# Kernel tuning notes

Measured on AMD Instinct MI355X. Metric: run time of the kernel, lower is better.

## Reference

```python
import jax, jax.numpy as jnp
import numpy as np

NUM_HEADS = 16

def setup_inputs() -> dict:
    key = jax.random.key(0)
    ks = jax.random.split(key, 5)
    b, n, d = 2, 2048, 1024
    s = 0.02
    return {
        "x": jax.random.normal(ks[0], (b, n, d), jnp.float32),
        "wq": jax.random.normal(ks[1], (d, d), jnp.float32) * s,
        "wk": jax.random.normal(ks[2], (d, d), jnp.float32) * s,
        "wv": jax.random.normal(ks[3], (d, d), jnp.float32) * s,
        "wo": jax.random.normal(ks[4], (d, d), jnp.float32) * s,
        "bo": jnp.zeros((d,), jnp.float32),
    }

def reference(x, wq, wk, wv, wo, bo):
    b, n, c = x.shape
    h = NUM_HEADS
    hd = c // h
    scale = hd ** -0.5
    # qkv projections (qkv_bias=False); torch Linear computes x @ W.T
    def split_heads(t):
        return t.reshape(b, n, h, hd).transpose(0, 2, 1, 3)  # b h n d
    q = split_heads(x @ wq.T)
    k = split_heads(x @ wk.T)
    v = split_heads(x @ wv.T)
    dots = jnp.einsum('bhid,bhjd->bhij', q, k) * scale
    attn = jax.nn.softmax(dots, axis=-1)  # attn_drop=0 -> identity
    out = jnp.einsum('bhij,bhjd->bhid', attn, v)
    out = out.transpose(0, 2, 1, 3).reshape(b, n, c)
    out = out @ wo.T + bo  # proj_drop=0 -> identity
    return out
```

## Files before the change

kernel.cpp:

```cpp
#include <hip/hip_runtime.h>
#include <hip/hip_bf16.h>

typedef float f32x4 __attribute__((ext_vector_type(4)));
typedef short short8 __attribute__((ext_vector_type(8)));
typedef short short4v __attribute__((ext_vector_type(4)));

#define MFMA(a, b, c) __builtin_amdgcn_mfma_f32_16x16x32_bf16((a), (b), (c), 0, 0, 0)

#if __has_builtin(__builtin_amdgcn_mfma_f32_16x16x16_bf16)
#define MFMA16(a, b, c) __builtin_amdgcn_mfma_f32_16x16x16_bf16((a), (b), (c), 0, 0, 0)
#elif __has_builtin(__builtin_amdgcn_mfma_f32_16x16x16bf16_1k)
#define MFMA16(a, b, c) __builtin_amdgcn_mfma_f32_16x16x16bf16_1k((a), (b), (c), 0, 0, 0)
#else
static __device__ __forceinline__ f32x4 mfma16_asm(short4v a, short4v b, f32x4 c) {
    asm volatile("v_mfma_f32_16x16x16_bf16 %0, %1, %2, %0" : "+v"(c) : "v"(a), "v"(b));
    return c;
}
#define MFMA16(a, b, c) mfma16_asm((a), (b), (c))
#endif

#if __has_builtin(__builtin_amdgcn_exp2f)
#define EXP2(x) __builtin_amdgcn_exp2f(x)
#else
#define EXP2(x) exp2f(x)
#endif

#define B_  2
#define N_  2048
#define C_  1024
#define H_  16
#define HD_ 64
#define M_  (B_ * N_)

#define QSCALE 0.18033688011112042f

typedef const __attribute__((address_space(1))) void* gp_t;
typedef __attribute__((address_space(3))) void* sp_t;
#define GLL16(g, s) __builtin_amdgcn_global_load_lds((gp_t)(const void*)(g), (sp_t)(void*)(s), 16, 0, 0)

__device__ __forceinline__ short f2bf(float f) {
    union { float fv; unsigned u; } v; v.fv = f;
    unsigned r = v.u + 0x7fffu + ((v.u >> 16) & 1u);
    return (short)(r >> 16);
}
__device__ __forceinline__ unsigned pack_rne(float a, float b) {
    return (unsigned)(unsigned short)f2bf(a) | ((unsigned)(unsigned short)f2bf(b) << 16);
}

__global__ __launch_bounds__(256) void convert_kernel(
    const float* __restrict__ x,  const float* __restrict__ wq,
    const float* __restrict__ wk, const float* __restrict__ wv,
    const float* __restrict__ wo, short* __restrict__ dst)
{
    size_t e = ((size_t)blockIdx.x * 256 + threadIdx.x) * 8;
    const float* src; size_t off;
    if (e < 4194304)      { src = x;  off = e; }
    else if (e < 5242880) { src = wq; off = e - 4194304; }
    else if (e < 6291456) { src = wk; off = e - 5242880; }
    else if (e < 7340032) { src = wv; off = e - 6291456; }
    else                  { src = wo; off = e - 7340032; }
    float4 a = *(const float4*)(src + off);
    float4 b = *(const float4*)(src + off + 4);
    short8 s;
    s[0] = f2bf(a.x); s[1] = f2bf(a.y); s[2] = f2bf(a.z); s[3] = f2bf(a.w);
    s[4] = f2bf(b.x); s[5] = f2bf(b.y); s[6] = f2bf(b.z); s[7] = f2bf(b.w);
    *(short8*)(dst + e) = s;
}

__global__ __launch_bounds__(256) void qkv_gemm(
    const short* __restrict__ xb, const short* __restrict__ Wb,
    short* __restrict__ Qb, short* __restrict__ Kb, short* __restrict__ Vt)
{
    const int m0 = blockIdx.x * 128;
    const int n0 = blockIdx.y * 128;
    __shared__ short As[128 * 32];
    __shared__ short Bs[128 * 32];
    const int tid  = threadIdx.x;
    const int wave = tid >> 6, lane = tid & 63;
    const int quad = lane >> 4, l16 = lane & 15;
    const int wr = (wave >> 1) * 64, wc = (wave & 1) * 64;

    f32x4 acc[4][4] = {};

    for (int kk = 0; kk < C_; kk += 32) {
        __syncthreads();
        #pragma unroll
        for (int it = 0; it < 2; ++it) {
            int f = (it * 256 + tid) * 8;
            int row = f >> 5, col = f & 31;
            GLL16(xb + (size_t)(m0 + row) * C_ + kk + col, &As[f]);
            GLL16(Wb + (size_t)(n0 + row) * C_ + kk + col, &Bs[f]);
        }
        __syncthreads();
        short8 af[4], bf[4];
        #pragma unroll
        for (int mi = 0; mi < 4; ++mi) af[mi] = *(const short8*)&As[(wr + mi * 16 + l16) * 32 + quad * 8];
        #pragma unroll
        for (int ni = 0; ni < 4; ++ni) bf[ni] = *(const short8*)&Bs[(wc + ni * 16 + l16) * 32 + quad * 8];
        #pragma unroll
        for (int mi = 0; mi < 4; ++mi)
        #pragma unroll
        for (int ni = 0; ni < 4; ++ni)
            acc[mi][ni] = MFMA(af[mi], bf[ni], acc[mi][ni]);
    }

    const int which = n0 >> 10;
    const int nb = n0 & 1023;
    #pragma unroll
    for (int mi = 0; mi < 4; ++mi)
    #pragma unroll
    for (int ni = 0; ni < 4; ++ni)
    #pragma unroll
    for (int r = 0; r < 4; ++r) {
        int m  = m0 + wr + mi * 16 + quad * 4 + r;
        int cc = nb + wc + ni * 16 + l16;
        float av = acc[mi][ni][r];
        if (which == 0) av *= QSCALE;
        short bv = f2bf(av);
        int b = m >> 11, ns = m & (N_ - 1);
        int h = cc >> 6, d = cc & 63;
        size_t bh = (size_t)(b * H_ + h);
        if (which == 0)      Qb[(bh * N_ + ns) * HD_ + d] = bv;
        else if (which == 1) Kb[(bh * N_ + ns) * HD_ + d] = bv;
        else                 Vt[(bh * HD_ + d) * N_ + ns] = bv;
    }
}

__global__ __launch_bounds__(256, 2) void attn_kernel(
    const short* __restrict__ Qb, const short* __restrict__ Kb,
    const short* __restrict__ Vt, short* __restrict__ Ob)
{
    const int bh = blockIdx.y;
    const int b = bh >> 4, h = bh & (H_ - 1);
    const int i0 = blockIdx.x * 128;
    __shared__ short Qs[128 * 72];
    __shared__ short Ks[64 * 72];
    __shared__ short Vs[64 * 72];
    const int tid  = threadIdx.x;
    const int wave = tid >> 6, lane = tid & 63;
    const int quad = lane >> 4, l16 = lane & 15;

    const short* Qg = Qb + ((size_t)bh * N_ + i0) * HD_;
    const short* Kg = Kb + (size_t)bh * N_ * HD_;
    const short* Vg = Vt + (size_t)bh * HD_ * N_;

    #pragma unroll
    for (int it = 0; it < 4; ++it) {
        int e = tid + it * 256;
        int row = e >> 3, c8 = e & 7;
        *(uint4*)&Qs[row * 72 + c8 * 8] = *(const uint4*)(Qg + row * HD_ + c8 * 8);
    }
    __syncthreads();
    short8 qf[2][2];
    #pragma unroll
    for (int s = 0; s < 2; ++s) {
        qf[s][0] = *(const short8*)&Qs[(wave * 32 + s * 16 + l16) * 72 +      quad * 8];
        qf[s][1] = *(const short8*)&Qs[(wave * 32 + s * 16 + l16) * 72 + 32 + quad * 8];
    }

    f32x4 o[2][4] = {};
    float lrow[2] = {0.f, 0.f};

    for (int j0 = 0; j0 < N_; j0 += 64) {
        __syncthreads();
        #pragma unroll
        for (int it = 0; it < 2; ++it) {
            int e = tid + it * 256;
            int row = e >> 3, c8 = e & 7;
            *(uint4*)&Ks[row * 72 + c8 * 8] = *(const uint4*)(Kg + (size_t)(j0 + row) * HD_ + c8 * 8);
            *(uint4*)&Vs[row * 72 + c8 * 8] = *(const uint4*)(Vg + (size_t)row * N_ + j0 + c8 * 8);
        }
        __syncthreads();

        #pragma unroll
        for (int ni = 0; ni < 4; ++ni) {
            short8 kf0 = *(const short8*)&Ks[(ni * 16 + l16) * 72 +      quad * 8];
            short8 kf1 = *(const short8*)&Ks[(ni * 16 + l16) * 72 + 32 + quad * 8];
            short4v pp[2];
            #pragma unroll
            for (int s = 0; s < 2; ++s) {
                f32x4 st = {0.f, 0.f, 0.f, 0.f};
                st = MFMA(kf0, qf[s][0], st);
                st = MFMA(kf1, qf[s][1], st);
                union { float f; unsigned u; } c0, c1, c2, c3;
                c0.f = EXP2(st[0]); c1.f = EXP2(st[1]);
                c2.f = EXP2(st[2]); c3.f = EXP2(st[3]);
                lrow[s] += (c0.f + c1.f) + (c2.f + c3.f);
                unsigned w0 = (c0.u >> 16) | (c1.u & 0xffff0000u);
                unsigned w1 = (c2.u >> 16) | (c3.u & 0xffff0000u);
                union { unsigned u[2]; short4v s4; } pk;
                pk.u[0] = w0; pk.u[1] = w1;
                pp[s] = pk.s4;
            }
            #pragma unroll
            for (int di = 0; di < 4; ++di) {
                short4v vf = *(const short4v*)&Vs[(di * 16 + l16) * 72 + ni * 16 + quad * 4];
                o[0][di] = MFMA16(vf, pp[0], o[0][di]);
                o[1][di] = MFMA16(vf, pp[1], o[1][di]);
            }
        }
    }

    #pragma unroll
    for (int s = 0; s < 2; ++s) {
        float l = lrow[s];
        l += __shfl_xor(l, 16, 64);
        l += __shfl_xor(l, 32, 64);
        float inv = 1.f / l;
        int ig = i0 + wave * 32 + s * 16 + l16;
        size_t base = ((size_t)(b * N_ + ig)) * C_ + h * HD_;
        #pragma unroll
        for (int di = 0; di < 4; ++di) {
            unsigned p01 = pack_rne(o[s][di][0] * inv, o[s][di][1] * inv);
            unsigned p23 = pack_rne(o[s][di][2] * inv, o[s][di][3] * inv);
            *(unsigned*)&Ob[base + di * 16 + quad * 4]     = p01;
            *(unsigned*)&Ob[base + di * 16 + quad * 4 + 2] = p23;
        }
    }
}

__global__ __launch_bounds__(256) void proj_gemm(
    const short* __restrict__ Ob, const short* __restrict__ wob,
    const float* __restrict__ bo, float* __restrict__ out)
{
    const int m0 = blockIdx.x * 64;
    const int n0 = blockIdx.y * 128;
    __shared__ short As[64 * 32];
    __shared__ short Bs[128 * 32];
    const int tid  = threadIdx.x;
    const int wave = tid >> 6, lane = tid & 63;
    const int quad = lane >> 4, l16 = lane & 15;
    const int wr = (wave >> 1) * 32, wc = (wave & 1) * 64;

    f32x4 acc[2][4] = {};

    for (int kk = 0; kk < C_; kk += 32) {
        __syncthreads();
        {
            int f = tid * 8;
            int row = f >> 5, col = f & 31;
            GLL16(Ob + (size_t)(m0 + row) * C_ + kk + col, &As[f]);
        }
        #pragma unroll
        for (int it = 0; it < 2; ++it) {
            int f = (it * 256 + tid) * 8;
            int row = f >> 5, col = f & 31;
            GLL16(wob + (size_t)(n0 + row) * C_ + kk + col, &Bs[f]);
        }
        __syncthreads();
        short8 af[2], bf[4];
        #pragma unroll
        for (int mi = 0; mi < 2; ++mi) af[mi] = *(const short8*)&As[(wr + mi * 16 + l16) * 32 + quad * 8];
        #pragma unroll
        for (int ni = 0; ni < 4; ++ni) bf[ni] = *(const short8*)&Bs[(wc + ni * 16 + l16) * 32 + quad * 8];
        #pragma unroll
        for (int mi = 0; mi < 2; ++mi)
        #pragma unroll
        for (int ni = 0; ni < 4; ++ni)
            acc[mi][ni] = MFMA(af[mi], bf[ni], acc[mi][ni]);
    }

    #pragma unroll
    for (int mi = 0; mi < 2; ++mi)
    #pragma unroll
    for (int ni = 0; ni < 4; ++ni)
    #pragma unroll
    for (int r = 0; r < 4; ++r) {
        int m = m0 + wr + mi * 16 + quad * 4 + r;
        int c = n0 + wc + ni * 16 + l16;
        out[(size_t)m * C_ + c] = acc[mi][ni][r] + bo[c];
    }
}

extern "C" void kernel_launch(void* const* d_in, const int* in_sizes, int n_in,
                              void* d_out, int out_size, void* d_ws, size_t ws_size,
                              hipStream_t stream) {
    const float* x  = (const float*)d_in[0];
    const float* wq = (const float*)d_in[1];
    const float* wk = (const float*)d_in[2];
    const float* wv = (const float*)d_in[3];
    const float* wo = (const float*)d_in[4];
    const float* bo = (const float*)d_in[5];
    float* out = (float*)d_out;

    short* xb  = (short*)d_ws;
    short* Wb  = xb  + 4194304;
    short* wob = Wb  + 3145728;
    short* Qb  = wob + 1048576;
    short* Kb  = Qb  + 4194304;
    short* Vt  = Kb  + 4194304;
    short* Obuf= Vt  + 4194304;

    dim3 blk(256);
    convert_kernel<<<4096, blk, 0, stream>>>(x, wq, wk, wv, wo, xb);
    qkv_gemm<<<dim3(M_ / 128, 3072 / 128), blk, 0, stream>>>(xb, Wb, Qb, Kb, Vt);
    attn_kernel<<<dim3(N_ / 128, B_ * H_), blk, 0, stream>>>(Qb, Kb, Vt, Obuf);
    proj_gemm<<<dim3(M_ / 64, C_ / 128), blk, 0, stream>>>(Obuf, wob, bo, out);
}
```

Baseline: 213.3 us.

## Restage attention P through LDS with XOR swizzle and register-prefetch K/V tiles

The attention kernel replaces the 16x16x16 PV MFMAs with 16x16x32 MFMAs by writing the exp'd probabilities into LDS (reusing the Q buffer) and reloading them in the operand layout. Q/K/V LDS tiles switch from padded rows to an XOR-swizzled layout to avoid bank conflicts, and the next K/V tile is prefetched into registers during the current iteration. The QKV GEMM swaps operand roles for the V block so that Vt stores are contiguous along the sequence. In exchange, there is an extra LDS round trip for P and more register pressure from the prefetch, and the output write becomes 2-byte scattered stores.

```diff
diff --git a/kernel.cpp b/kernel.cpp
--- a/kernel.cpp
+++ b/kernel.cpp
@@ -3,21 +3,8 @@
 
 typedef float f32x4 __attribute__((ext_vector_type(4)));
 typedef short short8 __attribute__((ext_vector_type(8)));
-typedef short short4v __attribute__((ext_vector_type(4)));
 
 #define MFMA(a, b, c) __builtin_amdgcn_mfma_f32_16x16x32_bf16((a), (b), (c), 0, 0, 0)
-
-#if __has_builtin(__builtin_amdgcn_mfma_f32_16x16x16_bf16)
-#define MFMA16(a, b, c) __builtin_amdgcn_mfma_f32_16x16x16_bf16((a), (b), (c), 0, 0, 0)
-#elif __has_builtin(__builtin_amdgcn_mfma_f32_16x16x16bf16_1k)
-#define MFMA16(a, b, c) __builtin_amdgcn_mfma_f32_16x16x16bf16_1k((a), (b), (c), 0, 0, 0)
-#else
-static __device__ __forceinline__ f32x4 mfma16_asm(short4v a, short4v b, f32x4 c) {
-    asm volatile("v_mfma_f32_16x16x16_bf16 %0, %1, %2, %0" : "+v"(c) : "v"(a), "v"(b));
-    return c;
-}
-#define MFMA16(a, b, c) mfma16_asm((a), (b), (c))
-#endif
 
 #if __has_builtin(__builtin_amdgcn_exp2f)
 #define EXP2(x) __builtin_amdgcn_exp2f(x)
@@ -42,9 +29,6 @@
     union { float fv; unsigned u; } v; v.fv = f;
     unsigned r = v.u + 0x7fffu + ((v.u >> 16) & 1u);
     return (short)(r >> 16);
-}
-__device__ __forceinline__ unsigned pack_rne(float a, float b) {
-    return (unsigned)(unsigned short)f2bf(a) | ((unsigned)(unsigned short)f2bf(b) << 16);
 }
 
 __global__ __launch_bounds__(256) void convert_kernel(
@@ -79,6 +63,10 @@
     const int wave = tid >> 6, lane = tid & 63;
     const int quad = lane >> 4, l16 = lane & 15;
     const int wr = (wave >> 1) * 64, wc = (wave & 1) * 64;
+    const int which = n0 >> 10;
+
+    const short* Fa = (which == 2) ? Bs : As;
+    const short* Fb = (which == 2) ? As : Bs;
 
     f32x4 acc[4][4] = {};
 
@@ -94,9 +82,9 @@
         __syncthreads();
         short8 af[4], bf[4];
         #pragma unroll
-        for (int mi = 0; mi < 4; ++mi) af[mi] = *(const short8*)&As[(wr + mi * 16 + l16) * 32 + quad * 8];
-        #pragma unroll
-        for (int ni = 0; ni < 4; ++ni) bf[ni] = *(const short8*)&Bs[(wc + ni * 16 + l16) * 32 + quad * 8];
+        for (int mi = 0; mi < 4; ++mi) af[mi] = *(const short8*)&Fa[(wr + mi * 16 + l16) * 32 + quad * 8];
+        #pragma unroll
+        for (int ni = 0; ni < 4; ++ni) bf[ni] = *(const short8*)&Fb[(wc + ni * 16 + l16) * 32 + quad * 8];
         #pragma unroll
         for (int mi = 0; mi < 4; ++mi)
         #pragma unroll
@@ -104,25 +92,38 @@
             acc[mi][ni] = MFMA(af[mi], bf[ni], acc[mi][ni]);
     }
 
-    const int which = n0 >> 10;
     const int nb = n0 & 1023;
-    #pragma unroll
-    for (int mi = 0; mi < 4; ++mi)
-    #pragma unroll
-    for (int ni = 0; ni < 4; ++ni)
-    #pragma unroll
-    for (int r = 0; r < 4; ++r) {
-        int m  = m0 + wr + mi * 16 + quad * 4 + r;
-        int cc = nb + wc + ni * 16 + l16;
-        float av = acc[mi][ni][r];
-        if (which == 0) av *= QSCALE;
-        short bv = f2bf(av);
-        int b = m >> 11, ns = m & (N_ - 1);
-        int h = cc >> 6, d = cc & 63;
-        size_t bh = (size_t)(b * H_ + h);
-        if (which == 0)      Qb[(bh * N_ + ns) * HD_ + d] = bv;
-        else if (which == 1) Kb[(bh * N_ + ns) * HD_ + d] = bv;
-        else                 Vt[(bh * HD_ + d) * N_ + ns] = bv;
+    if (which == 2) {
+        #pragma unroll
+        for (int mi = 0; mi < 4; ++mi)
+        #pragma unroll
+        for (int ni = 0; ni < 4; ++ni)
+        #pragma unroll
+        for (int r = 0; r < 4; ++r) {
+            int cc = nb + wr + mi * 16 + quad * 4 + r;
+            int m  = m0 + wc + ni * 16 + l16;
+            int bb = m >> 11, ns = m & (N_ - 1);
+            int h = cc >> 6, d = cc & 63;
+            Vt[(((size_t)(bb * H_ + h)) * HD_ + d) * N_ + ns] = f2bf(acc[mi][ni][r]);
+        }
+    } else {
+        #pragma unroll
+        for (int mi = 0; mi < 4; ++mi)
+        #pragma unroll
+        for (int ni = 0; ni < 4; ++ni)
+        #pragma unroll
+        for (int r = 0; r < 4; ++r) {
+            int m  = m0 + wr + mi * 16 + quad * 4 + r;
+            int cc = nb + wc + ni * 16 + l16;
+            float av = acc[mi][ni][r];
+            if (which == 0) av *= QSCALE;
+            short bv = f2bf(av);
+            int bb = m >> 11, ns = m & (N_ - 1);
+            int h = cc >> 6, d = cc & 63;
+            size_t bh = (size_t)(bb * H_ + h);
+            if (which == 0) Qb[(bh * N_ + ns) * HD_ + d] = bv;
+            else            Kb[(bh * N_ + ns) * HD_ + d] = bv;
+        }
     }
 }
 
@@ -133,12 +134,14 @@
     const int bh = blockIdx.y;
     const int b = bh >> 4, h = bh & (H_ - 1);
     const int i0 = blockIdx.x * 128;
-    __shared__ short Qs[128 * 72];
-    __shared__ short Ks[64 * 72];
-    __shared__ short Vs[64 * 72];
+    __shared__ short Qs[128 * 64];
+    __shared__ short Ks[64 * 64];
+    __shared__ short Vs[64 * 64];
+    short* const Ps = Qs;
     const int tid  = threadIdx.x;
     const int wave = tid >> 6, lane = tid & 63;
     const int quad = lane >> 4, l16 = lane & 15;
+    const int sw = l16 & 7;
 
     const short* Qg = Qb + ((size_t)bh * N_ + i0) * HD_;
     const short* Kg = Kb + (size_t)bh * N_ * HD_;
@@ -148,35 +151,53 @@
     for (int it = 0; it < 4; ++it) {
         int e = tid + it * 256;
         int row = e >> 3, c8 = e & 7;
-        *(uint4*)&Qs[row * 72 + c8 * 8] = *(const uint4*)(Qg + row * HD_ + c8 * 8);
+        *(uint4*)&Qs[row * 64 + ((c8 ^ (row & 7)) * 8)] = *(const uint4*)(Qg + row * HD_ + c8 * 8);
     }
     __syncthreads();
     short8 qf[2][2];
     #pragma unroll
     for (int s = 0; s < 2; ++s) {
-        qf[s][0] = *(const short8*)&Qs[(wave * 32 + s * 16 + l16) * 72 +      quad * 8];
-        qf[s][1] = *(const short8*)&Qs[(wave * 32 + s * 16 + l16) * 72 + 32 + quad * 8];
-    }
+        int row = (wave * 32 + s * 16 + l16) * 64;
+        qf[s][0] = *(const short8*)&Qs[row + ((quad ^ sw) * 8)];
+        qf[s][1] = *(const short8*)&Qs[row + (((quad + 4) ^ sw) * 8)];
+    }
+    __syncthreads();
 
     f32x4 o[2][4] = {};
     float lrow[2] = {0.f, 0.f};
 
+    uint4 kr[2], vr[2];
+    #pragma unroll
+    for (int it = 0; it < 2; ++it) {
+        int e = tid + it * 256, row = e >> 3, c8 = e & 7;
+        kr[it] = *(const uint4*)(Kg + (size_t)row * HD_ + c8 * 8);
+        vr[it] = *(const uint4*)(Vg + (size_t)row * N_ + c8 * 8);
+    }
+
     for (int j0 = 0; j0 < N_; j0 += 64) {
         __syncthreads();
         #pragma unroll
         for (int it = 0; it < 2; ++it) {
-            int e = tid + it * 256;
-            int row = e >> 3, c8 = e & 7;
-            *(uint4*)&Ks[row * 72 + c8 * 8] = *(const uint4*)(Kg + (size_t)(j0 + row) * HD_ + c8 * 8);
-            *(uint4*)&Vs[row * 72 + c8 * 8] = *(const uint4*)(Vg + (size_t)row * N_ + j0 + c8 * 8);
+            int e = tid + it * 256, row = e >> 3, c8 = e & 7;
+            int sc = (c8 ^ (row & 7)) * 8;
+            *(uint4*)&Ks[row * 64 + sc] = kr[it];
+            *(uint4*)&Vs[row * 64 + sc] = vr[it];
+        }
+        if (j0 + 64 < N_) {
+            #pragma unroll
+            for (int it = 0; it < 2; ++it) {
+                int e = tid + it * 256, row = e >> 3, c8 = e & 7;
+                kr[it] = *(const uint4*)(Kg + (size_t)(j0 + 64 + row) * HD_ + c8 * 8);
+                vr[it] = *(const uint4*)(Vg + (size_t)row * N_ + j0 + 64 + c8 * 8);
+            }
         }
         __syncthreads();
 
         #pragma unroll
         for (int ni = 0; ni < 4; ++ni) {
-            short8 kf0 = *(const short8*)&Ks[(ni * 16 + l16) * 72 +      quad * 8];
-            short8 kf1 = *(const short8*)&Ks[(ni * 16 + l16) * 72 + 32 + quad * 8];
-            short4v pp[2];
+            int krow = (ni * 16 + l16) * 64;
+            short8 kf0 = *(const short8*)&Ks[krow + ((quad ^ sw) * 8)];
+            short8 kf1 = *(const short8*)&Ks[krow + (((quad + 4) ^ sw) * 8)];
             #pragma unroll
             for (int s = 0; s < 2; ++s) {
                 f32x4 st = {0.f, 0.f, 0.f, 0.f};
@@ -188,15 +209,25 @@
                 lrow[s] += (c0.f + c1.f) + (c2.f + c3.f);
                 unsigned w0 = (c0.u >> 16) | (c1.u & 0xffff0000u);
                 unsigned w1 = (c2.u >> 16) | (c3.u & 0xffff0000u);
-                union { unsigned u[2]; short4v s4; } pk;
-                pk.u[0] = w0; pk.u[1] = w1;
-                pp[s] = pk.s4;
+                int irow = (wave * 32 + s * 16 + l16) * 64;
+                int chunk = (ni * 2 + (quad >> 1)) ^ sw;
+                *(uint2*)&Ps[irow + chunk * 8 + (quad & 1) * 4] = make_uint2(w0, w1);
             }
-            #pragma unroll
-            for (int di = 0; di < 4; ++di) {
-                short4v vf = *(const short4v*)&Vs[(di * 16 + l16) * 72 + ni * 16 + quad * 4];
-                o[0][di] = MFMA16(vf, pp[0], o[0][di]);
-                o[1][di] = MFMA16(vf, pp[1], o[1][di]);
+        }
+
+        #pragma unroll
+        for (int ks = 0; ks < 2; ++ks) {
+            int kc = ((ks * 4 + quad) ^ sw) * 8;
+            short8 vfr[4];
+            #pragma unroll
+            for (int di = 0; di < 4; ++di)
+                vfr[di] = *(const short8*)&Vs[(di * 16 + l16) * 64 + kc];
+            #pragma unroll
+            for (int s = 0; s < 2; ++s) {
+                short8 pf = *(const short8*)&Ps[(wave * 32 + s * 16 + l16) * 64 + kc];
+                #pragma unroll
+                for (int di = 0; di < 4; ++di)
+                    o[s][di] = MFMA(pf, vfr[di], o[s][di]);
             }
         }
     }
@@ -206,15 +237,14 @@
         float l = lrow[s];
         l += __shfl_xor(l, 16, 64);
         l += __shfl_xor(l, 32, 64);
-        float inv = 1.f / l;
-        int ig = i0 + wave * 32 + s * 16 + l16;
-        size_t base = ((size_t)(b * N_ + ig)) * C_ + h * HD_;
-        #pragma unroll
-        for (int di = 0; di < 4; ++di) {
-            unsigned p01 = pack_rne(o[s][di][0] * inv, o[s][di][1] * inv);
-            unsigned p23 = pack_rne(o[s][di][2] * inv, o[s][di][3] * inv);
-            *(unsigned*)&Ob[base + di * 16 + quad * 4]     = p01;
-            *(unsigned*)&Ob[base + di * 16 + quad * 4 + 2] = p23;
+        #pragma unroll
+        for (int r = 0; r < 4; ++r) {
+            float inv = 1.f / __shfl(l, quad * 4 + r, 64);
+            int ig = i0 + wave * 32 + s * 16 + quad * 4 + r;
+            size_t base = ((size_t)(b * N_ + ig)) * C_ + h * HD_;
+            #pragma unroll
+            for (int di = 0; di < 4; ++di)
+                Ob[base + di * 16 + l16] = f2bf(o[s][di][r] * inv);
         }
     }
 }
```

Result: slower. 233.9 us (+9.7%).

## Double K-step per barrier in GEMMs and transpose V tile for coalesced stores

Applied to the files above, without the earlier changes.

Both GEMM kernels now load two 32-wide K slices per iteration into separate LDS buffers, which halves the number of __syncthreads barriers and loop iterations. In the QKV GEMM, blocks producing V swap the A and B operands so the accumulator comes out transposed. That lets the transposed Vt store write along the sequence dimension with adjacent lanes instead of strided scattered writes. LDS use per block doubles, which may lower occupancy.

```diff
diff --git a/kernel.cpp b/kernel.cpp
--- a/kernel.cpp
+++ b/kernel.cpp
@@ -73,56 +73,79 @@
 {
     const int m0 = blockIdx.x * 128;
     const int n0 = blockIdx.y * 128;
-    __shared__ short As[128 * 32];
-    __shared__ short Bs[128 * 32];
+    __shared__ short As0[128 * 32], As1[128 * 32];
+    __shared__ short Bs0[128 * 32], Bs1[128 * 32];
     const int tid  = threadIdx.x;
     const int wave = tid >> 6, lane = tid & 63;
     const int quad = lane >> 4, l16 = lane & 15;
     const int wr = (wave >> 1) * 64, wc = (wave & 1) * 64;
+    const int which = n0 >> 10;
 
     f32x4 acc[4][4] = {};
 
-    for (int kk = 0; kk < C_; kk += 32) {
+    for (int kk = 0; kk < C_; kk += 64) {
         __syncthreads();
         #pragma unroll
         for (int it = 0; it < 2; ++it) {
             int f = (it * 256 + tid) * 8;
             int row = f >> 5, col = f & 31;
-            GLL16(xb + (size_t)(m0 + row) * C_ + kk + col, &As[f]);
-            GLL16(Wb + (size_t)(n0 + row) * C_ + kk + col, &Bs[f]);
-        }
-        __syncthreads();
-        short8 af[4], bf[4];
-        #pragma unroll
-        for (int mi = 0; mi < 4; ++mi) af[mi] = *(const short8*)&As[(wr + mi * 16 + l16) * 32 + quad * 8];
-        #pragma unroll
-        for (int ni = 0; ni < 4; ++ni) bf[ni] = *(const short8*)&Bs[(wc + ni * 16 + l16) * 32 + quad * 8];
+            GLL16(xb + (size_t)(m0 + row) * C_ + kk +      col, &As0[f]);
+            GLL16(xb + (size_t)(m0 + row) * C_ + kk + 32 + col, &As1[f]);
+            GLL16(Wb + (size_t)(n0 + row) * C_ + kk +      col, &Bs0[f]);
+            GLL16(Wb + (size_t)(n0 + row) * C_ + kk + 32 + col, &Bs1[f]);
+        }
+        __syncthreads();
+        #pragma unroll
+        for (int kc = 0; kc < 2; ++kc) {
+            const short* Sa = kc ? As1 : As0;
+            const short* Sb = kc ? Bs1 : Bs0;
+            const short* Fa = (which == 2) ? Sb : Sa;
+            const short* Fb = (which == 2) ? Sa : Sb;
+            short8 af[4], bf[4];
+            #pragma unroll
+            for (int mi = 0; mi < 4; ++mi) af[mi] = *(const short8*)&Fa[(wr + mi * 16 + l16) * 32 + quad * 8];
+            #pragma unroll
+            for (int ni = 0; ni < 4; ++ni) bf[ni] = *(const short8*)&Fb[(wc + ni * 16 + l16) * 32 + quad * 8];
+            #pragma unroll
+            for (int mi = 0; mi < 4; ++mi)
+            #pragma unroll
+            for (int ni = 0; ni < 4; ++ni)
+                acc[mi][ni] = MFMA(af[mi], bf[ni], acc[mi][ni]);
+        }
+    }
+
+    const int nb = n0 & 1023;
+    if (which == 2) {
         #pragma unroll
         for (int mi = 0; mi < 4; ++mi)
         #pragma unroll
         for (int ni = 0; ni < 4; ++ni)
-            acc[mi][ni] = MFMA(af[mi], bf[ni], acc[mi][ni]);
-    }
-
-    const int which = n0 >> 10;
-    const int nb = n0 & 1023;
-    #pragma unroll
-    for (int mi = 0; mi < 4; ++mi)
-    #pragma unroll
-    for (int ni = 0; ni < 4; ++ni)
-    #pragma unroll
-    for (int r = 0; r < 4; ++r) {
-        int m  = m0 + wr + mi * 16 + quad * 4 + r;
-        int cc = nb + wc + ni * 16 + l16;
-        float av = acc[mi][ni][r];
-        if (which == 0) av *= QSCALE;
-        short bv = f2bf(av);
-        int b = m >> 11, ns = m & (N_ - 1);
-        int h = cc >> 6, d = cc & 63;
-        size_t bh = (size_t)(b * H_ + h);
-        if (which == 0)      Qb[(bh * N_ + ns) * HD_ + d] = bv;
-        else if (which == 1) Kb[(bh * N_ + ns) * HD_ + d] = bv;
-        else                 Vt[(bh * HD_ + d) * N_ + ns] = bv;
+        #pragma unroll
+        for (int r = 0; r < 4; ++r) {
+            int cc = nb + wr + mi * 16 + quad * 4 + r;
+            int m  = m0 + wc + ni * 16 + l16;
+            int bb = m >> 11, ns = m & (N_ - 1);
+            int h = cc >> 6, d = cc & 63;
+            Vt[(((size_t)(bb * H_ + h)) * HD_ + d) * N_ + ns] = f2bf(acc[mi][ni][r]);
+        }
+    } else {
+        #pragma unroll
+        for (int mi = 0; mi < 4; ++mi)
+        #pragma unroll
+        for (int ni = 0; ni < 4; ++ni)
+        #pragma unroll
+        for (int r = 0; r < 4; ++r) {
+            int m  = m0 + wr + mi * 16 + quad * 4 + r;
+            int cc = nb + wc + ni * 16 + l16;
+            float av = acc[mi][ni][r];
+            if (which == 0) av *= QSCALE;
+            short bv = f2bf(av);
+            int bb = m >> 11, ns = m & (N_ - 1);
+            int h = cc >> 6, d = cc & 63;
+            size_t bh = (size_t)(bb * H_ + h);
+            if (which == 0) Qb[(bh * N_ + ns) * HD_ + d] = bv;
+            else            Kb[(bh * N_ + ns) * HD_ + d] = bv;
+        }
     }
 }
 
@@ -225,8 +248,8 @@
 {
     const int m0 = blockIdx.x * 64;
     const int n0 = blockIdx.y * 128;
-    __shared__ short As[64 * 32];
-    __shared__ short Bs[128 * 32];
+    __shared__ short As0[64 * 32], As1[64 * 32];
+    __shared__ short Bs0[128 * 32], Bs1[128 * 32];
     const int tid  = threadIdx.x;
     const int wave = tid >> 6, lane = tid & 63;
     const int quad = lane >> 4, l16 = lane & 15;
@@ -234,30 +257,37 @@
 
     f32x4 acc[2][4] = {};
 
-    for (int kk = 0; kk < C_; kk += 32) {
+    for (int kk = 0; kk < C_; kk += 64) {
         __syncthreads();
         {
             int f = tid * 8;
             int row = f >> 5, col = f & 31;
-            GLL16(Ob + (size_t)(m0 + row) * C_ + kk + col, &As[f]);
+            GLL16(Ob + (size_t)(m0 + row) * C_ + kk +      col, &As0[f]);
+            GLL16(Ob + (size_t)(m0 + row) * C_ + kk + 32 + col, &As1[f]);
         }
         #pragma unroll
         for (int it = 0; it < 2; ++it) {
             int f = (it * 256 + tid) * 8;
             int row = f >> 5, col = f & 31;
-            GLL16(wob + (size_t)(n0 + row) * C_ + kk + col, &Bs[f]);
-        }
-        __syncthreads();
-        short8 af[2], bf[4];
-        #pragma unroll
-        for (int mi = 0; mi < 2; ++mi) af[mi] = *(const short8*)&As[(wr + mi * 16 + l16) * 32 + quad * 8];
-        #pragma unroll
-        for (int ni = 0; ni < 4; ++ni) bf[ni] = *(const short8*)&Bs[(wc + ni * 16 + l16) * 32 + quad * 8];
-        #pragma unroll
-        for (int mi = 0; mi < 2; ++mi)
-        #pragma unroll
-        for (int ni = 0; ni < 4; ++ni)
-            acc[mi][ni] = MFMA(af[mi], bf[ni], acc[mi][ni]);
+            GLL16(wob + (size_t)(n0 + row) * C_ + kk +      col, &Bs0[f]);
+            GLL16(wob + (size_t)(n0 + row) * C_ + kk + 32 + col, &Bs1[f]);
+        }
+        __syncthreads();
+        #pragma unroll
+        for (int kc = 0; kc < 2; ++kc) {
+            const short* Sa = kc ? As1 : As0;
+            const short* Sb = kc ? Bs1 : Bs0;
+            short8 af[2], bf[4];
+            #pragma unroll
+            for (int mi = 0; mi < 2; ++mi) af[mi] = *(const short8*)&Sa[(wr + mi * 16 + l16) * 32 + quad * 8];
+            #pragma unroll
+            for (int ni = 0; ni < 4; ++ni) bf[ni] = *(const short8*)&Sb[(wc + ni * 16 + l16) * 32 + quad * 8];
+            #pragma unroll
+            for (int mi = 0; mi < 2; ++mi)
+            #pragma unroll
+            for (int ni = 0; ni < 4; ++ni)
+                acc[mi][ni] = MFMA(af[mi], bf[ni], acc[mi][ni]);
+        }
     }
 
     #pragma unroll
```

After: 217.1 us. No clear change (+1.8%).

## Double-buffer K/V tiles with direct global-to-LDS loads and XOR swizzle

Applied to the files above, without the earlier changes.

The attention kernel now fetches K and V tiles straight from global memory into shared memory with GLL16, into two buffers. The next tile is prefetched while the current one is consumed, which cuts the loop to one barrier per iteration. Row padding (stride 72) is replaced by an XOR swizzle on the column chunk, so LDS reads stay conflict-free without wasted space. In exchange, shared memory for K/V doubles, which may affect occupancy, and correctness depends on the barrier also waiting for the async loads to finish.

```diff
diff --git a/kernel.cpp b/kernel.cpp
--- a/kernel.cpp
+++ b/kernel.cpp
@@ -117,9 +117,9 @@
         float av = acc[mi][ni][r];
         if (which == 0) av *= QSCALE;
         short bv = f2bf(av);
-        int b = m >> 11, ns = m & (N_ - 1);
+        int bb = m >> 11, ns = m & (N_ - 1);
         int h = cc >> 6, d = cc & 63;
-        size_t bh = (size_t)(b * H_ + h);
+        size_t bh = (size_t)(bb * H_ + h);
         if (which == 0)      Qb[(bh * N_ + ns) * HD_ + d] = bv;
         else if (which == 1) Kb[(bh * N_ + ns) * HD_ + d] = bv;
         else                 Vt[(bh * HD_ + d) * N_ + ns] = bv;
@@ -133,72 +133,90 @@
     const int bh = blockIdx.y;
     const int b = bh >> 4, h = bh & (H_ - 1);
     const int i0 = blockIdx.x * 128;
-    __shared__ short Qs[128 * 72];
-    __shared__ short Ks[64 * 72];
-    __shared__ short Vs[64 * 72];
+    __shared__ short Qs[128 * 64];
+    __shared__ short Ks[2][64 * 64];
+    __shared__ short Vs[2][64 * 64];
     const int tid  = threadIdx.x;
     const int wave = tid >> 6, lane = tid & 63;
     const int quad = lane >> 4, l16 = lane & 15;
+    const int sw = l16 & 7;
 
     const short* Qg = Qb + ((size_t)bh * N_ + i0) * HD_;
     const short* Kg = Kb + (size_t)bh * N_ * HD_;
     const short* Vg = Vt + (size_t)bh * HD_ * N_;
 
+    const int row0 = tid >> 3,        c0 = (tid & 7) ^ (row0 & 7);
+    const int row1 = row0 + 32,       c1 = (tid & 7) ^ (row1 & 7);
+    const short* KgA0 = Kg + row0 * HD_ + c0 * 8;
+    const short* KgA1 = Kg + row1 * HD_ + c1 * 8;
+    const short* VgA0 = Vg + (size_t)row0 * N_ + c0 * 8;
+    const short* VgA1 = Vg + (size_t)row1 * N_ + c1 * 8;
+
     #pragma unroll
     for (int it = 0; it < 4; ++it) {
-        int e = tid + it * 256;
-        int row = e >> 3, c8 = e & 7;
-        *(uint4*)&Qs[row * 72 + c8 * 8] = *(const uint4*)(Qg + row * HD_ + c8 * 8);
-    }
+        int s = it * 256 + tid;
+        int row = s >> 3, c = (s & 7) ^ (row & 7);
+        GLL16(Qg + row * HD_ + c * 8, &Qs[s * 8]);
+    }
+    GLL16(KgA0, &Ks[0][tid * 8]);
+    GLL16(KgA1, &Ks[0][(tid + 256) * 8]);
+    GLL16(VgA0, &Vs[0][tid * 8]);
+    GLL16(VgA1, &Vs[0][(tid + 256) * 8]);
     __syncthreads();
+
     short8 qf[2][2];
     #pragma unroll
     for (int s = 0; s < 2; ++s) {
-        qf[s][0] = *(const short8*)&Qs[(wave * 32 + s * 16 + l16) * 72 +      quad * 8];
-        qf[s][1] = *(const short8*)&Qs[(wave * 32 + s * 16 + l16) * 72 + 32 + quad * 8];
+        int row = (wave * 32 + s * 16 + l16) * 64;
+        qf[s][0] = *(const short8*)&Qs[row + ((quad ^ sw) * 8)];
+        qf[s][1] = *(const short8*)&Qs[row + (((quad + 4) ^ sw) * 8)];
     }
 
     f32x4 o[2][4] = {};
     float lrow[2] = {0.f, 0.f};
 
-    for (int j0 = 0; j0 < N_; j0 += 64) {
-        __syncthreads();
-        #pragma unroll
-        for (int it = 0; it < 2; ++it) {
-            int e = tid + it * 256;
-            int row = e >> 3, c8 = e & 7;
-            *(uint4*)&Ks[row * 72 + c8 * 8] = *(const uint4*)(Kg + (size_t)(j0 + row) * HD_ + c8 * 8);
-            *(uint4*)&Vs[row * 72 + c8 * 8] = *(const uint4*)(Vg + (size_t)row * N_ + j0 + c8 * 8);
-        }
-        __syncthreads();
+    for (int jt = 0; jt < N_ / 64; ++jt) {
+        const int cur = jt & 1;
+        if (jt + 1 < N_ / 64) {
+            int j1 = (jt + 1) * 64;
+            GLL16(KgA0 + (size_t)j1 * HD_, &Ks[cur ^ 1][tid * 8]);
+            GLL16(KgA1 + (size_t)j1 * HD_, &Ks[cur ^ 1][(tid + 256) * 8]);
+            GLL16(VgA0 + j1, &Vs[cur ^ 1][tid * 8]);
+            GLL16(VgA1 + j1, &Vs[cur ^ 1][(tid + 256) * 8]);
+        }
+        const short* Kc = Ks[cur];
+        const short* Vc = Vs[cur];
 
         #pragma unroll
         for (int ni = 0; ni < 4; ++ni) {
-            short8 kf0 = *(const short8*)&Ks[(ni * 16 + l16) * 72 +      quad * 8];
-            short8 kf1 = *(const short8*)&Ks[(ni * 16 + l16) * 72 + 32 + quad * 8];
+            int krow = (ni * 16 + l16) * 64;
+            short8 kf0 = *(const short8*)&Kc[krow + ((quad ^ sw) * 8)];
+            short8 kf1 = *(const short8*)&Kc[krow + (((quad + 4) ^ sw) * 8)];
             short4v pp[2];
             #pragma unroll
             for (int s = 0; s < 2; ++s) {
                 f32x4 st = {0.f, 0.f, 0.f, 0.f};
                 st = MFMA(kf0, qf[s][0], st);
                 st = MFMA(kf1, qf[s][1], st);
-                union { float f; unsigned u; } c0, c1, c2, c3;
-                c0.f = EXP2(st[0]); c1.f = EXP2(st[1]);
-                c2.f = EXP2(st[2]); c3.f = EXP2(st[3]);
-                lrow[s] += (c0.f + c1.f) + (c2.f + c3.f);
-                unsigned w0 = (c0.u >> 16) | (c1.u & 0xffff0000u);
-                unsigned w1 = (c2.u >> 16) | (c3.u & 0xffff0000u);
+                union { float f; unsigned u; } e0, e1, e2, e3;
+                e0.f = EXP2(st[0]); e1.f = EXP2(st[1]);
+                e2.f = EXP2(st[2]); e3.f = EXP2(st[3]);
+                lrow[s] += (e0.f + e1.f) + (e2.f + e3.f);
+                unsigned w0 = (e0.u >> 16) | (e1.u & 0xffff0000u);
+                unsigned w1 = (e2.u >> 16) | (e3.u & 0xffff0000u);
                 union { unsigned u[2]; short4v s4; } pk;
                 pk.u[0] = w0; pk.u[1] = w1;
                 pp[s] = pk.s4;
             }
             #pragma unroll
             for (int di = 0; di < 4; ++di) {
-                short4v vf = *(const short4v*)&Vs[(di * 16 + l16) * 72 + ni * 16 + quad * 4];
+                int vrow = (di * 16 + l16) * 64;
+                short4v vf = *(const short4v*)&Vc[vrow + (((ni * 2 + (quad >> 1)) ^ sw) * 8) + (quad & 1) * 4];
                 o[0][di] = MFMA16(vf, pp[0], o[0][di]);
                 o[1][di] = MFMA16(vf, pp[1], o[1][di]);
             }
         }
+        __syncthreads();
     }
 
     #pragma unroll
```

Measured after the change: 193.9 us. 9.1% less time.
